# Kernel optimization log

Measured on AMD Instinct MI355X. Metric: run time of the kernel, lower is better.

The kernel has to match this reference:

```python
import jax, jax.numpy as jnp
import numpy as np

H, D = 8, 16            # num_heads, head_size
IN = H * D              # hgt_in_dim = 128
NT, ET = 3, 4           # node types, edge types (hard-coded in module)
N_DRUG, N_DIS, N_PROT = 10000, 10000, 30000
N = N_DRUG + N_DIS + N_PROT
E = 400000
LAYERS = 2
SQRT_D = float(np.sqrt(D))

# homogeneous node-type vector (presorted by type, as dgl.to_homogeneous yields)
NTYPE = jnp.concatenate([
    jnp.zeros(N_DRUG, jnp.int32),
    jnp.ones(N_DIS, jnp.int32),
    jnp.full((N_PROT,), 2, jnp.int32),
])


def typed_linear(x, types, W):
    # x: (M, in), W: (T, in, out), types: (M,) -> y[m] = x[m] @ W[types[m]]
    out = jnp.zeros((x.shape[0], W.shape[2]), x.dtype)
    for t in range(W.shape[0]):
        out = out + jnp.where((types == t)[:, None], x @ W[t], 0.0)
    return out


def hgt_conv(x, src, dst, etype, Wk, Wq, Wv, Wa, rel_att, rel_msg, pri, skip):
    # type-specific K/Q/V projections
    k = typed_linear(x, NTYPE, Wk).reshape(N, H, D)
    q = typed_linear(x, NTYPE, Wq).reshape(N, H, D)
    v = typed_linear(x, NTYPE, Wv).reshape(N, H, D)
    ke, qe, ve = k[src], q[dst], v[src]          # (E, H, D) gathers

    # per-edge-type relation transforms (vectorized over heads)
    kw = jnp.zeros_like(ke)
    mw = jnp.zeros_like(ve)
    for t in range(ET):
        sel = (etype == t)[:, None, None]
        kw = kw + jnp.where(sel, jnp.einsum('ehd,hdo->eho', ke, rel_att[:, t]), 0.0)
        mw = mw + jnp.where(sel, jnp.einsum('ehd,hdo->eho', ve, rel_msg[:, t]), 0.0)

    # attention logits: (kw . q) * relation_pri[head, etype] / sqrt(D)
    a = (kw * qe).sum(-1) * pri.T[etype] / SQRT_D  # (E, H)

    # edge softmax grouped by destination node, per head
    amax = jax.ops.segment_max(a, dst, num_segments=N)      # (N, H)
    ea = jnp.exp(a - amax[dst])
    esum = jax.ops.segment_sum(ea, dst, num_segments=N)
    attn = ea / esum[dst]                                   # (E, H)

    # weighted message aggregation (scatter-add over dst)
    m = mw * attn[..., None]                                 # (E, H, D)
    h = jax.ops.segment_sum(m, dst, num_segments=N).reshape(N, IN)

    # output projection (dropout = identity in eval) + sigmoid-skip residual
    h = typed_linear(h, NTYPE, Wa)
    alpha = jax.nn.sigmoid(skip)[NTYPE][:, None]
    return h * alpha + x * (1.0 - alpha)


def setup_inputs() -> dict:
    key = jax.random.key(0)
    ks = jax.random.split(key, 12)
    s = 0.05
    return {
        "drug_feature": jax.random.normal(ks[0], (N_DRUG, IN), jnp.float32),
        "disease_feature": jax.random.normal(ks[1], (N_DIS, IN), jnp.float32),
        "protein_feature": jax.random.normal(ks[2], (N_PROT, IN), jnp.float32),
        "src": jax.random.randint(ks[3], (E,), 0, N, dtype=jnp.int32),
        "dst": jax.random.randint(ks[4], (E,), 0, N, dtype=jnp.int32),
        "etype": jnp.sort(jax.random.randint(ks[5], (E,), 0, ET, dtype=jnp.int32)),
        "Wk": jax.random.normal(ks[6], (NT, IN, IN), jnp.float32) * s,
        "Wq": jax.random.normal(ks[7], (NT, IN, IN), jnp.float32) * s,
        "Wv": jax.random.normal(ks[8], (NT, IN, IN), jnp.float32) * s,
        "Wa": jax.random.normal(ks[9], (NT, IN, IN), jnp.float32) * s,
        "rel_att": jax.random.normal(ks[10], (H, ET, D, D), jnp.float32) * 0.1,
        "rel_msg": jax.random.normal(ks[11], (H, ET, D, D), jnp.float32) * 0.1,
        "pri": jnp.ones((H, ET), jnp.float32),
        "skip": jnp.ones((NT,), jnp.float32),
    }


def reference(drug_feature, disease_feature, protein_feature, src, dst, etype,
              Wk, Wq, Wv, Wa, rel_att, rel_msg, pri, skip):
    x = jnp.concatenate([drug_feature, disease_feature, protein_feature], axis=0)
    # ModuleList holds the SAME conv instance -> shared weights across layers
    for _ in range(LAYERS):
        x = hgt_conv(x, src, dst, etype, Wk, Wq, Wv, Wa, rel_att, rel_msg, pri, skip)
    return x
```

## Files before the change

kernel.cpp:

```cpp
#include <hip/hip_runtime.h>

#define N_NODE 50000
#define N_EDGE 400000
#define INF    128

#define FUSED_BLOCKS 1024

#define TILES0 313
#define TILES1 313
#define TILES2 938
#define PTILES 1564
#define PBLOCKS 391

typedef __bf16 bf16x8 __attribute__((ext_vector_type(8)));
typedef float  f32x4  __attribute__((ext_vector_type(4)));

__device__ __forceinline__ void seg_decode(int b, int& ty, int& base, int& nrows) {
  if (b < TILES0)            { ty = 0; base = b * 32;                      nrows = 10000 - base; }
  else if (b < TILES0+TILES1){ ty = 1; base = 10000 + (b - TILES0) * 32;   nrows = 20000 - base; }
  else                       { ty = 2; base = 20000 + (b - TILES0-TILES1)*32; nrows = 50000 - base; }
  if (nrows > 32) nrows = 32;
}

__device__ __forceinline__ float blo(unsigned u) { return __uint_as_float(u << 16); }
__device__ __forceinline__ float bhi(unsigned u) { return __uint_as_float(u & 0xffff0000u); }
__device__ __forceinline__ unsigned bpack(float lo, float hi) {
  unsigned a = __float_as_uint(lo), b = __float_as_uint(hi);
  a = (a + 0x7fffu + ((a >> 16) & 1u)) >> 16;
  b = (b + 0x7fffu + ((b >> 16) & 1u)) & 0xffff0000u;
  return a | b;
}
__device__ __forceinline__ unsigned short b16(float v) {
  unsigned u = __float_as_uint(v);
  return (unsigned short)((u + 0x7fffu + ((u >> 16) & 1u)) >> 16);
}
__device__ __forceinline__ bf16x8 ld_frag(const unsigned short* p) {
  uint4 u = *reinterpret_cast<const uint4*>(p);
  return __builtin_bit_cast(bf16x8, u);
}

__global__ __launch_bounds__(256) void k_concat(const float* __restrict__ dr,
                                                const float* __restrict__ di,
                                                const float* __restrict__ pr,
                                                float* __restrict__ x,
                                                unsigned short* __restrict__ xh) {
  for (int i = blockIdx.x * 256 + threadIdx.x; i < N_NODE * 32; i += 2048 * 256) {
    int row = i >> 5;
    float4 val;
    if (row < 10000)      val = ((const float4*)dr)[i];
    else if (row < 20000) val = ((const float4*)di)[i - 10000*32];
    else                  val = ((const float4*)pr)[i - 20000*32];
    ((float4*)x)[i] = val;
    ((uint2*)xh)[i] = make_uint2(bpack(val.x, val.y), bpack(val.z, val.w));
  }
}

__global__ __launch_bounds__(256) void k_count(const int* __restrict__ dst, int* __restrict__ deg) {
  int e = blockIdx.x * 256 + threadIdx.x;
  if (e < N_EDGE) atomicAdd(&deg[dst[e]], 1);
}

__global__ __launch_bounds__(1024) void k_scan(const int* __restrict__ deg,
                                               int* __restrict__ off, int* __restrict__ cur) {
  __shared__ int part[1024];
  int t = threadIdx.x;
  int c0 = t * 49;
  int c1 = c0 + 49; if (c1 > N_NODE) c1 = N_NODE;
  int s = 0;
  for (int i = c0; i < c1; ++i) s += deg[i];
  part[t] = s;
  __syncthreads();
  for (int ofs = 1; ofs < 1024; ofs <<= 1) {
    int v = (t >= ofs) ? part[t - ofs] : 0;
    __syncthreads();
    part[t] += v;
    __syncthreads();
  }
  int run = (t == 0) ? 0 : part[t - 1];
  for (int i = c0; i < c1; ++i) { off[i] = run; cur[i] = run; run += deg[i]; }
  if (t == 1023) off[N_NODE] = part[1023];
}

__global__ __launch_bounds__(256) void k_fill(const int* __restrict__ dst,
                                              const int* __restrict__ src,
                                              const int* __restrict__ etp,
                                              int* __restrict__ cur, int* __restrict__ est) {
  int e = blockIdx.x * 256 + threadIdx.x;
  if (e < N_EDGE) {
    int p = atomicAdd(&cur[dst[e]], 1);
    est[p] = (src[e] << 2) | etp[e];
  }
}

__global__ __launch_bounds__(256) void k_trmsg(const float* __restrict__ rm,
                                               float* __restrict__ AmT) {
  int i = blockIdx.x * 256 + threadIdx.x;
  int di = i & 15, doo = (i >> 4) & 15, ty = (i >> 8) & 3, hh = i >> 10;
  AmT[i] = rm[((hh * 4 + ty) * 16 + di) * 16 + doo];
}

__global__ __launch_bounds__(256) void k_twt(const float* __restrict__ Wk,
                                             const float* __restrict__ Wq,
                                             const float* __restrict__ Wv,
                                             const float* __restrict__ Wa,
                                             unsigned short* __restrict__ WT) {
  int idx = blockIdx.x * 256 + threadIdx.x;
  if (idx >= 196608) return;
  int mt = idx >> 14;
  int within = idx & 16383;
  int o = within >> 7, ii = within & 127;
  int mat = mt / 3, ty = mt % 3;
  const float* W = (mat == 0) ? Wk : (mat == 1) ? Wq : (mat == 2) ? Wv : Wa;
  WT[idx] = b16(W[ty * 16384 + ii * 128 + o]);
}

__global__ __launch_bounds__(256) void k_qkv(const unsigned short* __restrict__ xh,
                                             const unsigned short* __restrict__ WT,
                                             const float* __restrict__ rel_att,
                                             const float* __restrict__ pri,
                                             uint2* __restrict__ kvb,
                                             uint4* __restrict__ qab) {
  __shared__ unsigned short qsh[4][32][128];
  int w = threadIdx.x >> 6, l = threadIdx.x & 63;
  int r16 = l & 15, ks = l >> 4;
  int tile = blockIdx.x * 4 + w;
  int ty, base, wrows;
  seg_decode(tile, ty, base, wrows);
  int row0 = base;

  bf16x8 a[2][4];
#pragma unroll
  for (int st = 0; st < 2; ++st) {
    const unsigned short* xrow = xh + (size_t)(row0 + st * 16 + r16) * 128 + ks * 8;
#pragma unroll
    for (int kk = 0; kk < 4; ++kk) a[st][kk] = ld_frag(xrow + kk * 32);
  }

  const unsigned short* WK = WT + (size_t)(0 * 3 + ty) * 16384;
  const unsigned short* WQ = WT + (size_t)(1 * 3 + ty) * 16384;
  const unsigned short* WV = WT + (size_t)(2 * 3 + ty) * 16384;

#pragma unroll 1
  for (int ct = 0; ct < 8; ++ct) {
    int o = ct * 16 + r16;
    bf16x8 fbk[4], fbq[4], fbv[4];
#pragma unroll
    for (int kk = 0; kk < 4; ++kk) {
      fbk[kk] = ld_frag(WK + (size_t)o * 128 + ks * 8 + kk * 32);
      fbq[kk] = ld_frag(WQ + (size_t)o * 128 + ks * 8 + kk * 32);
      fbv[kk] = ld_frag(WV + (size_t)o * 128 + ks * 8 + kk * 32);
    }
#pragma unroll
    for (int st = 0; st < 2; ++st) {
      f32x4 ak = {0.f,0.f,0.f,0.f}, aq = {0.f,0.f,0.f,0.f}, av = {0.f,0.f,0.f,0.f};
#pragma unroll
      for (int kk = 0; kk < 4; ++kk) {
        ak = __builtin_amdgcn_mfma_f32_16x16x32_bf16(a[st][kk], fbk[kk], ak, 0, 0, 0);
        aq = __builtin_amdgcn_mfma_f32_16x16x32_bf16(a[st][kk], fbq[kk], aq, 0, 0, 0);
        av = __builtin_amdgcn_mfma_f32_16x16x32_bf16(a[st][kk], fbv[kk], av, 0, 0, 0);
      }
#pragma unroll
      for (int r = 0; r < 4; ++r) {
        int rrel = st * 16 + ks * 4 + r;
        float kn = __shfl_xor(ak[r], 1);
        float vn = __shfl_xor(av[r], 1);
        qsh[w][rrel][o] = b16(aq[r]);
        if (rrel < wrows && (l & 1) == 0) {
          size_t p = (size_t)(row0 + rrel);
          kvb[p * 64 + (o >> 1)] = make_uint2(bpack(ak[r], kn), bpack(av[r], vn));
        }
      }
    }
  }

  int h = l >> 3, j = l & 7;
  float4 prh = ((const float4*)pri)[h];
  float prs[4] = { prh.x * 0.25f, prh.y * 0.25f, prh.z * 0.25f, prh.w * 0.25f };
  for (int nd = 0; nd < wrows; ++nd) {
    unsigned u[8];
    *(uint4*)&u[0] = *(uint4*)&qsh[w][nd][h * 16 + 0];
    *(uint4*)&u[4] = *(uint4*)&qsh[w][nd][h * 16 + 8];
    float qf[16];
#pragma unroll
    for (int q2 = 0; q2 < 8; ++q2) { qf[2*q2] = blo(u[q2]); qf[2*q2+1] = bhi(u[q2]); }
    unsigned pk[4];
#pragma unroll
    for (int t4 = 0; t4 < 4; ++t4) {
      const float* Ar = rel_att + (((h * 4 + t4) * 16) + 2 * j) * 16;
      float ax = 0.f, ay = 0.f;
#pragma unroll
      for (int o = 0; o < 16; ++o) {
        ax += Ar[o] * qf[o];
        ay += Ar[16 + o] * qf[o];
      }
      pk[t4] = bpack(ax * prs[t4], ay * prs[t4]);
    }
    qab[(size_t)(row0 + nd) * 64 + l] = make_uint4(pk[0], pk[1], pk[2], pk[3]);
  }
}

__global__ __launch_bounds__(256)
__attribute__((amdgpu_waves_per_eu(4, 4)))
void k_fused(const uint2* __restrict__ kvb,
             const uint4* __restrict__ qab,
             const int* __restrict__ off,
             const int* __restrict__ est,
             const float* __restrict__ AmT,
             unsigned* __restrict__ hbh) {
  __shared__ float accs[4][4][128];
  int w = threadIdx.x >> 6, l = threadIdx.x & 63;
  int h = l >> 3, j = l & 7;

  for (int n = blockIdx.x * 4 + w; n < N_NODE; n += FUSED_BLOCKS * 4) {
    int o0 = off[n], o1 = off[n + 1];

    uint4 qu = qab[(size_t)n * 64 + l];
    float2 qa0 = make_float2(blo(qu.x), bhi(qu.x));
    float2 qa1 = make_float2(blo(qu.y), bhi(qu.y));
    float2 qa2 = make_float2(blo(qu.z), bhi(qu.z));
    float2 qa3 = make_float2(blo(qu.w), bhi(qu.w));

    float ssum = 0.f;
    float2 z = make_float2(0.f, 0.f);
    float2 at0 = z, at1 = z, at2 = z, at3 = z;

#define PROC(KV, TY, VALID) { \
    int ty = (TY) & 3; \
    float kx = blo((KV).x), ky = bhi((KV).x); \
    float2 qat = (ty==0)?qa0:(ty==1)?qa1:(ty==2)?qa2:qa3; \
    float part = kx*qat.x + ky*qat.y; \
    part += __shfl_xor(part, 1); \
    part += __shfl_xor(part, 2); \
    part += __shfl_xor(part, 4); \
    float wgt = (VALID) ? __expf(part) : 0.f; \
    ssum += wgt; \
    float vx = blo((KV).y), vy = bhi((KV).y); \
    float w0=(ty==0)?wgt:0.f, w1=(ty==1)?wgt:0.f, w2=(ty==2)?wgt:0.f, w3=(ty==3)?wgt:0.f; \
    at0.x += w0*vx; at0.y += w0*vy; \
    at1.x += w1*vx; at1.y += w1*vy; \
    at2.x += w2*vx; at2.y += w2*vy; \
    at3.x += w3*vx; at3.y += w3*vy; }

    for (int b0 = o0; b0 < o1; b0 += 64) {
      int cnt = o1 - b0; if (cnt > 64) cnt = 64;
      int stv = est[b0 + (l < cnt ? l : cnt - 1)];
      int t0 = __shfl(stv, 0);
      int t1 = __shfl(stv, 1 < cnt ? 1 : 0);
      uint2 kv0 = kvb[(size_t)(t0 >> 2) * 64 + l];
      uint2 kv1 = kvb[(size_t)(t1 >> 2) * 64 + l];
      for (int i = 0; i < cnt; i += 2) {
        bool more = (i + 2) < cnt;
        int n0 = 0, n1 = 0; uint2 kn0, kn1;
        if (more) {
          n0 = __shfl(stv, i + 2);
          n1 = __shfl(stv, (i + 3) < cnt ? (i + 3) : (i + 2));
          kn0 = kvb[(size_t)(n0 >> 2) * 64 + l];
          kn1 = kvb[(size_t)(n1 >> 2) * 64 + l];
        }
        PROC(kv0, t0, true)
        PROC(kv1, t1, (i + 1) < cnt)
        if (more) { t0 = n0; t1 = n1; kv0 = kn0; kv1 = kn1; }
      }
    }
#undef PROC

    float inv = (ssum > 0.f) ? 1.f / ssum : 0.f;
    at0.x *= inv; at0.y *= inv;
    at1.x *= inv; at1.y *= inv;
    at2.x *= inv; at2.y *= inv;
    at3.x *= inv; at3.y *= inv;

    ((float2*)&accs[w][0][0])[l] = at0;
    ((float2*)&accs[w][1][0])[l] = at1;
    ((float2*)&accs[w][2][0])[l] = at2;
    ((float2*)&accs[w][3][0])[l] = at3;

    float ox = 0.f, oy = 0.f;
#pragma unroll
    for (int ty = 0; ty < 4; ++ty) {
      const float4* AmR = (const float4*)(AmT + ((h * 4 + ty) * 16) * 16);
#pragma unroll
      for (int d4 = 0; d4 < 4; ++d4) {
        float4 ac = *((float4*)&accs[w][ty][h * 16 + d4 * 4]);
        float4 m0 = AmR[(2 * j) * 4 + d4];
        float4 m1 = AmR[(2 * j + 1) * 4 + d4];
        ox += m0.x * ac.x + m0.y * ac.y + m0.z * ac.z + m0.w * ac.w;
        oy += m1.x * ac.x + m1.y * ac.y + m1.z * ac.z + m1.w * ac.w;
      }
    }
    hbh[(size_t)n * 64 + l] = bpack(ox, oy);
  }
}

__global__ __launch_bounds__(256) void k_out(const unsigned short* __restrict__ hbh,
                                             const unsigned short* __restrict__ WT,
                                             const float* __restrict__ skipv,
                                             float* __restrict__ xio,
                                             unsigned short* __restrict__ xh,
                                             int write_xh) {
  int w = threadIdx.x >> 6, l = threadIdx.x & 63;
  int r16 = l & 15, ks = l >> 4;
  int tile = blockIdx.x * 4 + w;
  int ty, base, wrows;
  seg_decode(tile, ty, base, wrows);
  int row0 = base;

  bf16x8 a[2][4];
#pragma unroll
  for (int st = 0; st < 2; ++st) {
    const unsigned short* hrow = hbh + (size_t)(row0 + st * 16 + r16) * 128 + ks * 8;
#pragma unroll
    for (int kk = 0; kk < 4; ++kk) a[st][kk] = ld_frag(hrow + kk * 32);
  }

  const unsigned short* WA = WT + (size_t)(3 * 3 + ty) * 16384;
  float alpha = 1.f / (1.f + __expf(-skipv[ty]));
  float beta = 1.f - alpha;

#pragma unroll 1
  for (int ct = 0; ct < 8; ++ct) {
    int o = ct * 16 + r16;
    bf16x8 ba[4];
#pragma unroll
    for (int kk = 0; kk < 4; ++kk)
      ba[kk] = ld_frag(WA + (size_t)o * 128 + ks * 8 + kk * 32);
#pragma unroll
    for (int st = 0; st < 2; ++st) {
      f32x4 acc = {0.f,0.f,0.f,0.f};
#pragma unroll
      for (int kk = 0; kk < 4; ++kk)
        acc = __builtin_amdgcn_mfma_f32_16x16x32_bf16(a[st][kk], ba[kk], acc, 0, 0, 0);
#pragma unroll
      for (int r = 0; r < 4; ++r) {
        int rrel = st * 16 + ks * 4 + r;
        size_t p = (size_t)(row0 + rrel) * 128 + o;
        float nx = 0.f;
        if (rrel < wrows) {
          nx = acc[r] * alpha + xio[p] * beta;
          xio[p] = nx;
        }
        float nxn = __shfl_xor(nx, 1);
        if (write_xh && rrel < wrows && (l & 1) == 0)
          ((unsigned*)xh)[p >> 1] = bpack(nx, nxn);
      }
    }
  }
}

extern "C" void kernel_launch(void* const* d_in, const int* in_sizes, int n_in,
                              void* d_out, int out_size, void* d_ws, size_t ws_size,
                              hipStream_t stream) {
  const float* drug = (const float*)d_in[0];
  const float* dis  = (const float*)d_in[1];
  const float* prot = (const float*)d_in[2];
  const int* src    = (const int*)d_in[3];
  const int* dst    = (const int*)d_in[4];
  const int* etp    = (const int*)d_in[5];
  const float* Wk   = (const float*)d_in[6];
  const float* Wq   = (const float*)d_in[7];
  const float* Wv   = (const float*)d_in[8];
  const float* Wa   = (const float*)d_in[9];
  const float* rel_att = (const float*)d_in[10];
  const float* rel_msg = (const float*)d_in[11];
  const float* pri  = (const float*)d_in[12];
  const float* skip = (const float*)d_in[13];
  float* x = (float*)d_out;

  char* w = (char*)d_ws;
  uint2*          kvb = (uint2*)(w + 0);
  unsigned*       hbh = (unsigned*)(w + 25600000);
  uint4*          qab = (uint4*)(w + 38400000);
  unsigned short* xh  = (unsigned short*)(w + 89600000);
  unsigned short* WT  = (unsigned short*)(w + 102400000);
  float*          AmT = (float*)(w + 102793216);
  int*            off = (int*)(w + 102825984);
  int*            est = (int*)(w + 103026048);
  int*            deg = (int*)(w + 25600000);
  int*            cur = (int*)(w + 25800064);

  k_concat<<<2048, 256, 0, stream>>>(drug, dis, prot, x, xh);

  (void)hipMemsetAsync(deg, 0, N_NODE * sizeof(int), stream);
  (void)hipMemsetAsync(est + N_EDGE, 0, 64 * sizeof(int), stream);
  k_count<<<(N_EDGE + 255) / 256, 256, 0, stream>>>(dst, deg);
  k_scan<<<1, 1024, 0, stream>>>(deg, off, cur);
  k_fill<<<(N_EDGE + 255) / 256, 256, 0, stream>>>(dst, src, etp, cur, est);

  k_trmsg<<<32, 256, 0, stream>>>(rel_msg, AmT);
  k_twt<<<768, 256, 0, stream>>>(Wk, Wq, Wv, Wa, WT);

  for (int layer = 0; layer < 2; ++layer) {
    k_qkv<<<PBLOCKS, 256, 0, stream>>>(xh, WT, rel_att, pri, kvb, qab);
    k_fused<<<FUSED_BLOCKS, 256, 0, stream>>>(kvb, qab, off, est, AmT, hbh);
    k_out<<<PBLOCKS, 256, 0, stream>>>((const unsigned short*)hbh, WT, skip, x, xh,
                                       layer == 0 ? 1 : 0);
  }
}
```

Measured before the change: 795.5 us.

## Fuse setup kernels and merge layer-1 output projection with layer-2 QKV

Merges concat, degree count, weight transpose and rel_msg transpose into one multi-role setup kernel. The est padding memset moves into k_fill. The layer-1 output projection is fused with the layer-2 QKV projection: each wave keeps the updated x tile in shared memory as bf16 and feeds it straight into the K/Q/V MFMAs, so the xh round trip and one launch go away. This cuts kernel launches and global traffic. The cost is a larger fused kernel with more registers and shared memory, which may lower occupancy.

```diff
diff --git a/kernel.cpp b/kernel.cpp
--- a/kernel.cpp
+++ b/kernel.cpp
@@ -11,6 +11,12 @@
 #define TILES2 938
 #define PTILES 1564
 #define PBLOCKS 391
+
+#define SB_CONCAT 2048
+#define SB_COUNT  1563
+#define SB_TWT    768
+#define SB_TRMSG  32
+#define SB_TOTAL  (SB_CONCAT + SB_COUNT + SB_TWT + SB_TRMSG)
 
 typedef __bf16 bf16x8 __attribute__((ext_vector_type(8)));
 typedef float  f32x4  __attribute__((ext_vector_type(4)));
@@ -39,25 +45,49 @@
   return __builtin_bit_cast(bf16x8, u);
 }
 
-__global__ __launch_bounds__(256) void k_concat(const float* __restrict__ dr,
-                                                const float* __restrict__ di,
-                                                const float* __restrict__ pr,
-                                                float* __restrict__ x,
-                                                unsigned short* __restrict__ xh) {
-  for (int i = blockIdx.x * 256 + threadIdx.x; i < N_NODE * 32; i += 2048 * 256) {
-    int row = i >> 5;
-    float4 val;
-    if (row < 10000)      val = ((const float4*)dr)[i];
-    else if (row < 20000) val = ((const float4*)di)[i - 10000*32];
-    else                  val = ((const float4*)pr)[i - 20000*32];
-    ((float4*)x)[i] = val;
-    ((uint2*)xh)[i] = make_uint2(bpack(val.x, val.y), bpack(val.z, val.w));
-  }
-}
-
-__global__ __launch_bounds__(256) void k_count(const int* __restrict__ dst, int* __restrict__ deg) {
-  int e = blockIdx.x * 256 + threadIdx.x;
-  if (e < N_EDGE) atomicAdd(&deg[dst[e]], 1);
+__global__ __launch_bounds__(256) void k_setup(const float* __restrict__ dr,
+                                               const float* __restrict__ di,
+                                               const float* __restrict__ pr,
+                                               float* __restrict__ x,
+                                               unsigned short* __restrict__ xh,
+                                               const int* __restrict__ dst,
+                                               int* __restrict__ deg,
+                                               const float* __restrict__ Wk,
+                                               const float* __restrict__ Wq,
+                                               const float* __restrict__ Wv,
+                                               const float* __restrict__ Wa,
+                                               unsigned short* __restrict__ WT,
+                                               const float* __restrict__ rm,
+                                               float* __restrict__ AmT) {
+  int b = blockIdx.x;
+  if (b < SB_CONCAT) {
+    for (int i = b * 256 + threadIdx.x; i < N_NODE * 32; i += SB_CONCAT * 256) {
+      int row = i >> 5;
+      float4 val;
+      if (row < 10000)      val = ((const float4*)dr)[i];
+      else if (row < 20000) val = ((const float4*)di)[i - 10000*32];
+      else                  val = ((const float4*)pr)[i - 20000*32];
+      ((float4*)x)[i] = val;
+      ((uint2*)xh)[i] = make_uint2(bpack(val.x, val.y), bpack(val.z, val.w));
+    }
+  } else if (b < SB_CONCAT + SB_COUNT) {
+    int e = (b - SB_CONCAT) * 256 + threadIdx.x;
+    if (e < N_EDGE) atomicAdd(&deg[dst[e]], 1);
+  } else if (b < SB_CONCAT + SB_COUNT + SB_TWT) {
+    int idx = (b - SB_CONCAT - SB_COUNT) * 256 + threadIdx.x;
+    if (idx < 196608) {
+      int mt = idx >> 14;
+      int within = idx & 16383;
+      int o = within >> 7, ii = within & 127;
+      int mat = mt / 3, ty = mt % 3;
+      const float* W = (mat == 0) ? Wk : (mat == 1) ? Wq : (mat == 2) ? Wv : Wa;
+      WT[idx] = b16(W[ty * 16384 + ii * 128 + o]);
+    }
+  } else {
+    int i = (b - SB_CONCAT - SB_COUNT - SB_TWT) * 256 + threadIdx.x;
+    int di2 = i & 15, doo = (i >> 4) & 15, ty = (i >> 8) & 3, hh = i >> 10;
+    AmT[i] = rm[((hh * 4 + ty) * 16 + di2) * 16 + doo];
+  }
 }
 
 __global__ __launch_bounds__(1024) void k_scan(const int* __restrict__ deg,
@@ -89,29 +119,9 @@
   if (e < N_EDGE) {
     int p = atomicAdd(&cur[dst[e]], 1);
     est[p] = (src[e] << 2) | etp[e];
-  }
-}
-
-__global__ __launch_bounds__(256) void k_trmsg(const float* __restrict__ rm,
-                                               float* __restrict__ AmT) {
-  int i = blockIdx.x * 256 + threadIdx.x;
-  int di = i & 15, doo = (i >> 4) & 15, ty = (i >> 8) & 3, hh = i >> 10;
-  AmT[i] = rm[((hh * 4 + ty) * 16 + di) * 16 + doo];
-}
-
-__global__ __launch_bounds__(256) void k_twt(const float* __restrict__ Wk,
-                                             const float* __restrict__ Wq,
-                                             const float* __restrict__ Wv,
-                                             const float* __restrict__ Wa,
-                                             unsigned short* __restrict__ WT) {
-  int idx = blockIdx.x * 256 + threadIdx.x;
-  if (idx >= 196608) return;
-  int mt = idx >> 14;
-  int within = idx & 16383;
-  int o = within >> 7, ii = within & 127;
-  int mat = mt / 3, ty = mt % 3;
-  const float* W = (mat == 0) ? Wk : (mat == 1) ? Wq : (mat == 2) ? Wv : Wa;
-  WT[idx] = b16(W[ty * 16384 + ii * 128 + o]);
+  } else if (e < N_EDGE + 64) {
+    est[e] = 0;
+  }
 }
 
 __global__ __launch_bounds__(256) void k_qkv(const unsigned short* __restrict__ xh,
@@ -292,12 +302,15 @@
   }
 }
 
-__global__ __launch_bounds__(256) void k_out(const unsigned short* __restrict__ hbh,
-                                             const unsigned short* __restrict__ WT,
-                                             const float* __restrict__ skipv,
-                                             float* __restrict__ xio,
-                                             unsigned short* __restrict__ xh,
-                                             int write_xh) {
+__global__ __launch_bounds__(256) void k_outqkv(const unsigned short* __restrict__ hbh,
+                                                const unsigned short* __restrict__ WT,
+                                                const float* __restrict__ skipv,
+                                                const float* __restrict__ rel_att,
+                                                const float* __restrict__ pri,
+                                                float* __restrict__ xio,
+                                                uint2* __restrict__ kvb,
+                                                uint4* __restrict__ qab) {
+  __shared__ unsigned short qsh[4][32][136];
   int w = threadIdx.x >> 6, l = threadIdx.x & 63;
   int r16 = l & 15, ks = l >> 4;
   int tile = blockIdx.x * 4 + w;
@@ -305,6 +318,125 @@
   seg_decode(tile, ty, base, wrows);
   int row0 = base;
 
+  {
+    bf16x8 a[2][4];
+#pragma unroll
+    for (int st = 0; st < 2; ++st) {
+      const unsigned short* hrow = hbh + (size_t)(row0 + st * 16 + r16) * 128 + ks * 8;
+#pragma unroll
+      for (int kk = 0; kk < 4; ++kk) a[st][kk] = ld_frag(hrow + kk * 32);
+    }
+    const unsigned short* WA = WT + (size_t)(3 * 3 + ty) * 16384;
+    float alpha = 1.f / (1.f + __expf(-skipv[ty]));
+    float beta = 1.f - alpha;
+#pragma unroll 1
+    for (int ct = 0; ct < 8; ++ct) {
+      int o = ct * 16 + r16;
+      bf16x8 ba[4];
+#pragma unroll
+      for (int kk = 0; kk < 4; ++kk)
+        ba[kk] = ld_frag(WA + (size_t)o * 128 + ks * 8 + kk * 32);
+#pragma unroll
+      for (int st = 0; st < 2; ++st) {
+        f32x4 acc = {0.f,0.f,0.f,0.f};
+#pragma unroll
+        for (int kk = 0; kk < 4; ++kk)
+          acc = __builtin_amdgcn_mfma_f32_16x16x32_bf16(a[st][kk], ba[kk], acc, 0, 0, 0);
+#pragma unroll
+        for (int r = 0; r < 4; ++r) {
+          int rrel = st * 16 + ks * 4 + r;
+          size_t p = (size_t)(row0 + rrel) * 128 + o;
+          float nx = 0.f;
+          if (rrel < wrows) {
+            nx = acc[r] * alpha + xio[p] * beta;
+            xio[p] = nx;
+          }
+          qsh[w][rrel][o] = b16(nx);
+        }
+      }
+    }
+  }
+
+  bf16x8 a[2][4];
+#pragma unroll
+  for (int st = 0; st < 2; ++st)
+#pragma unroll
+    for (int kk = 0; kk < 4; ++kk)
+      a[st][kk] = ld_frag(&qsh[w][st * 16 + r16][ks * 8 + kk * 32]);
+
+  const unsigned short* WK = WT + (size_t)(0 * 3 + ty) * 16384;
+  const unsigned short* WQ = WT + (size_t)(1 * 3 + ty) * 16384;
+  const unsigned short* WV = WT + (size_t)(2 * 3 + ty) * 16384;
+#pragma unroll 1
+  for (int ct = 0; ct < 8; ++ct) {
+    int o = ct * 16 + r16;
+    bf16x8 fbk[4], fbq[4], fbv[4];
+#pragma unroll
+    for (int kk = 0; kk < 4; ++kk) {
+      fbk[kk] = ld_frag(WK + (size_t)o * 128 + ks * 8 + kk * 32);
+      fbq[kk] = ld_frag(WQ + (size_t)o * 128 + ks * 8 + kk * 32);
+      fbv[kk] = ld_frag(WV + (size_t)o * 128 + ks * 8 + kk * 32);
+    }
+#pragma unroll
+    for (int st = 0; st < 2; ++st) {
+      f32x4 ak = {0.f,0.f,0.f,0.f}, aq = {0.f,0.f,0.f,0.f}, av = {0.f,0.f,0.f,0.f};
+#pragma unroll
+      for (int kk = 0; kk < 4; ++kk) {
+        ak = __builtin_amdgcn_mfma_f32_16x16x32_bf16(a[st][kk], fbk[kk], ak, 0, 0, 0);
+        aq = __builtin_amdgcn_mfma_f32_16x16x32_bf16(a[st][kk], fbq[kk], aq, 0, 0, 0);
+        av = __builtin_amdgcn_mfma_f32_16x16x32_bf16(a[st][kk], fbv[kk], av, 0, 0, 0);
+      }
+#pragma unroll
+      for (int r = 0; r < 4; ++r) {
+        int rrel = st * 16 + ks * 4 + r;
+        float kn = __shfl_xor(ak[r], 1);
+        float vn = __shfl_xor(av[r], 1);
+        qsh[w][rrel][o] = b16(aq[r]);
+        if (rrel < wrows && (l & 1) == 0) {
+          size_t p = (size_t)(row0 + rrel);
+          kvb[p * 64 + (o >> 1)] = make_uint2(bpack(ak[r], kn), bpack(av[r], vn));
+        }
+      }
+    }
+  }
+
+  int h = l >> 3, j = l & 7;
+  float4 prh = ((const float4*)pri)[h];
+  float prs[4] = { prh.x * 0.25f, prh.y * 0.25f, prh.z * 0.25f, prh.w * 0.25f };
+  for (int nd = 0; nd < wrows; ++nd) {
+    unsigned u[8];
+    *(uint4*)&u[0] = *(uint4*)&qsh[w][nd][h * 16 + 0];
+    *(uint4*)&u[4] = *(uint4*)&qsh[w][nd][h * 16 + 8];
+    float qf[16];
+#pragma unroll
+    for (int q2 = 0; q2 < 8; ++q2) { qf[2*q2] = blo(u[q2]); qf[2*q2+1] = bhi(u[q2]); }
+    unsigned pk[4];
+#pragma unroll
+    for (int t4 = 0; t4 < 4; ++t4) {
+      const float* Ar = rel_att + (((h * 4 + t4) * 16) + 2 * j) * 16;
+      float ax = 0.f, ay = 0.f;
+#pragma unroll
+      for (int o = 0; o < 16; ++o) {
+        ax += Ar[o] * qf[o];
+        ay += Ar[16 + o] * qf[o];
+      }
+      pk[t4] = bpack(ax * prs[t4], ay * prs[t4]);
+    }
+    qab[(size_t)(row0 + nd) * 64 + l] = make_uint4(pk[0], pk[1], pk[2], pk[3]);
+  }
+}
+
+__global__ __launch_bounds__(256) void k_out(const unsigned short* __restrict__ hbh,
+                                             const unsigned short* __restrict__ WT,
+                                             const float* __restrict__ skipv,
+                                             float* __restrict__ xio) {
+  int w = threadIdx.x >> 6, l = threadIdx.x & 63;
+  int r16 = l & 15, ks = l >> 4;
+  int tile = blockIdx.x * 4 + w;
+  int ty, base, wrows;
+  seg_decode(tile, ty, base, wrows);
+  int row0 = base;
+
   bf16x8 a[2][4];
 #pragma unroll
   for (int st = 0; st < 2; ++st) {
@@ -333,15 +465,10 @@
 #pragma unroll
       for (int r = 0; r < 4; ++r) {
         int rrel = st * 16 + ks * 4 + r;
-        size_t p = (size_t)(row0 + rrel) * 128 + o;
-        float nx = 0.f;
         if (rrel < wrows) {
-          nx = acc[r] * alpha + xio[p] * beta;
-          xio[p] = nx;
+          size_t p = (size_t)(row0 + rrel) * 128 + o;
+          xio[p] = acc[r] * alpha + xio[p] * beta;
         }
-        float nxn = __shfl_xor(nx, 1);
-        if (write_xh && rrel < wrows && (l & 1) == 0)
-          ((unsigned*)xh)[p >> 1] = bpack(nx, nxn);
       }
     }
   }
@@ -378,21 +505,16 @@
   int*            deg = (int*)(w + 25600000);
   int*            cur = (int*)(w + 25800064);
 
-  k_concat<<<2048, 256, 0, stream>>>(drug, dis, prot, x, xh);
-
   (void)hipMemsetAsync(deg, 0, N_NODE * sizeof(int), stream);
-  (void)hipMemsetAsync(est + N_EDGE, 0, 64 * sizeof(int), stream);
-  k_count<<<(N_EDGE + 255) / 256, 256, 0, stream>>>(dst, deg);
+  k_setup<<<SB_TOTAL, 256, 0, stream>>>(drug, dis, prot, x, xh, dst, deg,
+                                        Wk, Wq, Wv, Wa, WT, rel_msg, AmT);
   k_scan<<<1, 1024, 0, stream>>>(deg, off, cur);
-  k_fill<<<(N_EDGE + 255) / 256, 256, 0, stream>>>(dst, src, etp, cur, est);
-
-  k_trmsg<<<32, 256, 0, stream>>>(rel_msg, AmT);
-  k_twt<<<768, 256, 0, stream>>>(Wk, Wq, Wv, Wa, WT);
-
-  for (int layer = 0; layer < 2; ++layer) {
-    k_qkv<<<PBLOCKS, 256, 0, stream>>>(xh, WT, rel_att, pri, kvb, qab);
-    k_fused<<<FUSED_BLOCKS, 256, 0, stream>>>(kvb, qab, off, est, AmT, hbh);
-    k_out<<<PBLOCKS, 256, 0, stream>>>((const unsigned short*)hbh, WT, skip, x, xh,
-                                       layer == 0 ? 1 : 0);
-  }
-}
+  k_fill<<<(N_EDGE + 64 + 255) / 256, 256, 0, stream>>>(dst, src, etp, cur, est);
+
+  k_qkv<<<PBLOCKS, 256, 0, stream>>>(xh, WT, rel_att, pri, kvb, qab);
+  k_fused<<<FUSED_BLOCKS, 256, 0, stream>>>(kvb, qab, off, est, AmT, hbh);
+  k_outqkv<<<PBLOCKS, 256, 0, stream>>>((const unsigned short*)hbh, WT, skip,
+                                        rel_att, pri, x, kvb, qab);
+  k_fused<<<FUSED_BLOCKS, 256, 0, stream>>>(kvb, qab, off, est, AmT, hbh);
+  k_out<<<PBLOCKS, 256, 0, stream>>>((const unsigned short*)hbh, WT, skip, x);
+}
```

After: 779.8 us. 1.02x faster.
